# Kernel tuning notes

Hardware: AMD Instinct MI355X
Metric: run time of the kernel (lower is better)

Reference implementation:

```python
import jax, jax.numpy as jnp
import numpy as np

SCALE = 1.0 / (100.0 ** 0.5)  # module hard-codes QK / sqrt(100)


def setup_inputs() -> dict:
    key = jax.random.key(0)
    k1, k2, k3 = jax.random.split(key, 3)
    B, S, D = 8, 2048, 512
    head_size = 64
    x = jax.random.normal(k1, (B, S, D), dtype=jnp.float32)
    kernel = jax.random.normal(k2, (3, D, head_size), dtype=jnp.float32) * 0.02
    dense = jax.random.normal(k3, (D, D), dtype=jnp.float32) * 0.02
    return {"x": x, "kernel": kernel, "dense": dense, "heads": 8}


def reference(x, kernel, dense, heads):
    # All heads use the SAME kernel slices in the original loop, so each
    # iteration produces an identical V; compute once and tile.
    WQ = jnp.einsum('bsd,dh->bsh', x, kernel[0])  # [B,S,Hd]
    WK = jnp.einsum('bsd,dh->bsh', x, kernel[1])
    WV = jnp.einsum('bsd,dh->bsh', x, kernel[2])
    scores = jnp.einsum('bqh,bkh->bqk', WQ, WK) * SCALE  # [B,S,S]
    attn = jax.nn.softmax(scores, axis=-1)
    V = jnp.einsum('bqk,bkh->bqh', attn, WV)  # [B,S,Hd]
    out = jnp.tile(V, (1, 1, heads))  # concat of identical heads -> [B,S,heads*Hd]
    return jnp.einsum('bsf,fo->bso', out, dense)
```

## Files before the change

kernel.cpp:

```cpp
#include <hip/hip_runtime.h>
#include <math.h>


typedef __bf16 bf16;
typedef __bf16 bf16x4v __attribute__((ext_vector_type(4)));
typedef __bf16 bf16x8v __attribute__((ext_vector_type(8)));
typedef float f32x4 __attribute__((ext_vector_type(4)));

namespace {
constexpr int kS = 2048;
constexpr int kD = 512;
constexpr int kRows = 16384;
}

#define MFMA16(a, b, c) __builtin_amdgcn_mfma_f32_16x16x32_bf16((a), (b), (c), 0, 0, 0)

__global__ __launch_bounds__(256) void prep_kernel(const float* __restrict__ w,
                                                   const float* __restrict__ dense,
                                                   bf16* __restrict__ wtg,
                                                   bf16* __restrict__ drt) {
  const int bid = blockIdx.x, tid = threadIdx.x;
  __shared__ float T[64][65];

  if (bid < 24) {
    const int mat = bid >> 3, k0 = (bid & 7) * 64;
#pragma unroll
    for (int p = 0; p < 16; ++p) {
      int e = tid + p * 256;
      int r = e >> 6, n = e & 63;
      T[r][n] = w[mat * 32768 + (k0 + r) * 64 + n];
    }
    __syncthreads();
#pragma unroll
    for (int p = 0; p < 16; ++p) {
      int e = tid + p * 256;
      int n = e >> 6, c = e & 63;
      wtg[(size_t)mat * 32768 + (size_t)n * 512 + k0 + c] = (bf16)T[c][n];
    }
  } else {
    const int o0 = (bid - 24) * 64;
    const int oo = tid & 63, jg = tid >> 6;
    float a[16];
#pragma unroll
    for (int i = 0; i < 16; ++i) a[i] = 0.f;
#pragma unroll
    for (int h = 0; h < 8; ++h)
#pragma unroll
      for (int i = 0; i < 16; ++i)
        a[i] += dense[(size_t)(h * 64 + jg * 16 + i) * kD + o0 + oo];
#pragma unroll
    for (int i = 0; i < 16; ++i) T[oo][jg * 16 + i] = a[i];
    __syncthreads();
#pragma unroll
    for (int p = 0; p < 16; ++p) {
      int e = tid + p * 256;
      int r = e >> 6, j = e & 63;
      drt[(size_t)(o0 + r) * 64 + j] = (bf16)T[r][j];
    }
  }
}

__global__ __launch_bounds__(512) void proj_kernel(const float* __restrict__ x,
                                                   const bf16* __restrict__ wtg,
                                                   bf16* __restrict__ wq,
                                                   bf16* __restrict__ wk,
                                                   bf16* __restrict__ wvt) {
  const int bt = blockIdx.x;
  const int tid = threadIdx.x;
  const int w = tid >> 6, tx = tid & 15, quad = (tid >> 4) & 3;
  const int rt = w & 3, nh = w >> 2;
  const int row0 = bt * 64;

  __shared__ bf16 Xs[64 * 72];
  __shared__ bf16 Wts[3 * 64 * 72];

  f32x4 acc[6];
#pragma unroll
  for (int j = 0; j < 6; ++j) acc[j] = (f32x4){0.f, 0.f, 0.f, 0.f};

  const int xr0 = tid >> 4, xc4 = (tid & 15) * 4;
  const float* xb0 = &x[(size_t)(row0 + xr0) * kD + xc4];
  const float* xb1 = &x[(size_t)(row0 + xr0 + 32) * kD + xc4];
  const int wn = tid >> 3, wc8 = (tid & 7) * 8;
  const bf16* wb = &wtg[(size_t)wn * 512 + wc8];

  float4 xf0, xf1;
  uint4 wf0, wf1, wf2;
#define PROJ_ISSUE(K0)                        \
  do {                                        \
    xf0 = *(const float4*)(xb0 + (K0));       \
    xf1 = *(const float4*)(xb1 + (K0));       \
    wf0 = *(const uint4*)(wb + (K0));         \
    wf1 = *(const uint4*)(wb + 32768 + (K0)); \
    wf2 = *(const uint4*)(wb + 65536 + (K0)); \
  } while (0)

  PROJ_ISSUE(0);
  for (int k0 = 0; k0 < kD; k0 += 64) {
    __syncthreads();
    {
      bf16x4v h0 = {(bf16)xf0.x, (bf16)xf0.y, (bf16)xf0.z, (bf16)xf0.w};
      *(bf16x4v*)&Xs[xr0 * 72 + xc4] = h0;
      bf16x4v h1 = {(bf16)xf1.x, (bf16)xf1.y, (bf16)xf1.z, (bf16)xf1.w};
      *(bf16x4v*)&Xs[(xr0 + 32) * 72 + xc4] = h1;
      *(uint4*)&Wts[(0 * 64 + wn) * 72 + wc8] = wf0;
      *(uint4*)&Wts[(1 * 64 + wn) * 72 + wc8] = wf1;
      *(uint4*)&Wts[(2 * 64 + wn) * 72 + wc8] = wf2;
    }
    if (k0 + 64 < kD) PROJ_ISSUE(k0 + 64);
    __syncthreads();
#pragma unroll
    for (int s = 0; s < 2; ++s) {
      bf16x8v a = *(bf16x8v*)&Xs[(rt * 16 + tx) * 72 + s * 32 + quad * 8];
#pragma unroll
      for (int j = 0; j < 6; ++j) {
        int ntg = nh * 6 + j;
        bf16x8v bfr = *(bf16x8v*)&Wts[(ntg * 16 + tx) * 72 + s * 32 + quad * 8];
        acc[j] = MFMA16(a, bfr, acc[j]);
      }
    }
  }

#pragma unroll
  for (int j = 0; j < 6; ++j) {
    int ntg = nh * 6 + j, mat = ntg >> 2, nt = ntg & 3;
    if (mat < 2) {
      bf16* dst = mat ? wk : wq;
#pragma unroll
      for (int r = 0; r < 4; ++r) {
        int row_g = row0 + rt * 16 + quad * 4 + r;
        dst[(size_t)row_g * 64 + nt * 16 + tx] = (bf16)acc[j][r];
      }
    }
  }
  __syncthreads();
  bf16* Vt = Xs;
#pragma unroll
  for (int j = 0; j < 6; ++j) {
    int ntg = nh * 6 + j, mat = ntg >> 2, nt = ntg & 3;
    if (mat == 2) {
#pragma unroll
      for (int r = 0; r < 4; ++r)
        Vt[(nt * 16 + tx) * 72 + rt * 16 + quad * 4 + r] = (bf16)acc[j][r];
    }
  }
  __syncthreads();
  {
    int v = tid >> 3, seg = tid & 7;
    *(uint4*)&wvt[(size_t)v * kRows + row0 + seg * 8] =
        *(uint4*)&Vt[v * 72 + seg * 8];
  }
}

__global__ __launch_bounds__(512, 2) void flash_kernel(
    const bf16* __restrict__ wq, const bf16* __restrict__ wk,
    const bf16* __restrict__ wvt, const bf16* __restrict__ drt,
    float* __restrict__ out) {
  const int bid = blockIdx.x;
  const int b = bid & 7, qb = bid >> 3;
  const int q0 = qb * 32;
  const int tid = threadIdx.x;
  const int w = tid >> 6, tx = tid & 15, quad = (tid >> 4) & 3;

  __shared__ __align__(16) char lds[65536];
  __shared__ float Lsh[256];
  __shared__ __align__(16) bf16 vob[32 * 64];
  bf16* Psw = (bf16*)(lds + w * 8192);

  const bf16* wqb = wq + (size_t)(b * kS) * 64;
  const bf16* wkb = wk + (size_t)(b * kS) * 64;
  const bf16* wvb = wvt + b * kS;

  const int kc0 = (quad ^ (tx & 7)) * 8;
  const int kc1 = ((4 + quad) ^ (tx & 7)) * 8;
  const int h2 = (tx ^ (tx >> 2)) & 3;

  bf16x8v aq[2][2];
#pragma unroll
  for (int rt = 0; rt < 2; ++rt)
#pragma unroll
    for (int s = 0; s < 2; ++s)
      aq[rt][s] = *(const bf16x8v*)&wqb[(size_t)(q0 + rt * 16 + tx) * 64 +
                                        s * 32 + quad * 8];

  f32x4 oacc[2][4];
#pragma unroll
  for (int rt = 0; rt < 2; ++rt)
#pragma unroll
    for (int nt = 0; nt < 4; ++nt) oacc[rt][nt] = (f32x4){0.f, 0.f, 0.f, 0.f};
  float lsum[2][4] = {};

  const bf16* kfp = &wkb[(size_t)tx * 64 + quad * 8];
  const bf16* vfp = &wvb[(size_t)tx * kRows + quad * 8];

  for (int t = 0; t < 8; ++t) {
    const int k0 = (t * 8 + w) * 32;

    bf16x8v vb0 = *(const bf16x8v*)(vfp + (size_t)0 * 16 * kRows + k0);
    bf16x8v vb1 = *(const bf16x8v*)(vfp + (size_t)1 * 16 * kRows + k0);
    bf16x8v vb2 = *(const bf16x8v*)(vfp + (size_t)2 * 16 * kRows + k0);
    bf16x8v vb3 = *(const bf16x8v*)(vfp + (size_t)3 * 16 * kRows + k0);

#pragma unroll
    for (int nt = 0; nt < 2; ++nt) {
      const bf16* krow_p = kfp + (size_t)(k0 + nt * 16) * 64;
      bf16x8v b0 = *(const bf16x8v*)(krow_p);
      bf16x8v b1 = *(const bf16x8v*)(krow_p + 32);
#pragma unroll
      for (int rt = 0; rt < 2; ++rt) {
        f32x4 z = (f32x4){0.f, 0.f, 0.f, 0.f};
        z = MFMA16(aq[rt][0], b0, z);
        z = MFMA16(aq[rt][1], b1, z);
#pragma unroll
        for (int r = 0; r < 4; ++r) {
          float p = __expf(z[r] * 0.1f);
          lsum[rt][r] += p;
          int q = rt * 16 + quad * 4 + r;
          int chunk = nt * 2 + (tx >> 3);
          Psw[q * 32 + ((chunk ^ (r ^ quad)) * 8) + (tx & 7)] = (bf16)p;
        }
      }
    }

#pragma unroll
    for (int rt = 0; rt < 2; ++rt) {
      bf16x8v pa = *(bf16x8v*)&Psw[(rt * 16 + tx) * 32 + ((quad ^ h2) * 8)];
      oacc[rt][0] = MFMA16(pa, vb0, oacc[rt][0]);
      oacc[rt][1] = MFMA16(pa, vb1, oacc[rt][1]);
      oacc[rt][2] = MFMA16(pa, vb2, oacc[rt][2]);
      oacc[rt][3] = MFMA16(pa, vb3, oacc[rt][3]);
    }
  }

  __syncthreads();
  float* myO = (float*)(lds + w * 8192);
  float* myL = Lsh + w * 32;
#pragma unroll
  for (int rt = 0; rt < 2; ++rt)
#pragma unroll
    for (int nt = 0; nt < 4; ++nt)
#pragma unroll
      for (int r = 0; r < 4; ++r)
        myO[(rt * 16 + quad * 4 + r) * 64 + nt * 16 + tx] = oacc[rt][nt][r];
#pragma unroll
  for (int rt = 0; rt < 2; ++rt)
#pragma unroll
    for (int r = 0; r < 4; ++r) {
      float v = lsum[rt][r];
#pragma unroll
      for (int m = 1; m < 16; m <<= 1) v += __shfl_xor(v, m, 64);
      if (tx == 0) myL[rt * 16 + quad * 4 + r] = v;
    }
  __syncthreads();

#pragma unroll
  for (int p = 0; p < 4; ++p) {
    int e = tid + p * 512;
    int row = e >> 6, col = e & 63;
    float s = 0.f, lt = 0.f;
#pragma unroll
    for (int wv = 0; wv < 8; ++wv) {
      s += ((const float*)(lds + wv * 8192))[e];
      lt += Lsh[wv * 32 + row];
    }
    vob[row * 64 + (((col >> 3) ^ (row & 7)) * 8) + (col & 7)] = (bf16)(s / lt);
  }
  __syncthreads();

  bf16x8v av[2][2];
#pragma unroll
  for (int rt = 0; rt < 2; ++rt) {
    av[rt][0] = *(bf16x8v*)&vob[(rt * 16 + tx) * 64 + kc0];
    av[rt][1] = *(bf16x8v*)&vob[(rt * 16 + tx) * 64 + kc1];
  }

  float* OutS = (float*)lds;
#pragma unroll
  for (int c = 0; c < 2; ++c) {
    if (c) __syncthreads();
#pragma unroll
    for (int i = 0; i < 2; ++i) {
      const int ct = c * 16 + w * 2 + i;
      bf16x8v bd0 =
          *(const bf16x8v*)&drt[(size_t)(ct * 16 + tx) * 64 + quad * 8];
      bf16x8v bd1 =
          *(const bf16x8v*)&drt[(size_t)(ct * 16 + tx) * 64 + 32 + quad * 8];
#pragma unroll
      for (int rt = 0; rt < 2; ++rt) {
        f32x4 z = (f32x4){0.f, 0.f, 0.f, 0.f};
        z = MFMA16(av[rt][0], bd0, z);
        z = MFMA16(av[rt][1], bd1, z);
#pragma unroll
        for (int r = 0; r < 4; ++r)
          OutS[(rt * 16 + quad * 4 + r) * 260 + (w * 2 + i) * 16 + tx] = z[r];
      }
    }
    __syncthreads();
#pragma unroll
    for (int p = 0; p < 4; ++p) {
      int e = tid + p * 512;
      int row = e >> 6, seg = e & 63;
      *(float4*)&out[(size_t)(b * kS + q0 + row) * kD + c * 256 + seg * 4] =
          *(float4*)&OutS[row * 260 + seg * 4];
    }
  }
}

extern "C" void kernel_launch(void* const* d_in, const int* in_sizes, int n_in,
                              void* d_out, int out_size, void* d_ws,
                              size_t ws_size, hipStream_t stream) {
  const float* x = (const float*)d_in[0];
  const float* w = (const float*)d_in[1];
  const float* dense = (const float*)d_in[2];
  float* out = (float*)d_out;

  bf16* wq = (bf16*)d_ws;
  bf16* wk = wq + (size_t)kRows * 64;
  bf16* wvt = wk + (size_t)kRows * 64;
  bf16* wtg = wvt + (size_t)kRows * 64;
  bf16* drt = wtg + 98304;

  prep_kernel<<<32, 256, 0, stream>>>(w, dense, wtg, drt);
  proj_kernel<<<256, 512, 0, stream>>>(x, wtg, wq, wk, wvt);
  flash_kernel<<<512, 512, 0, stream>>>(wq, wk, wvt, drt, out);
}
```

Before: 140.2 us.

## Prefetch K tiles into swizzled per-wave LDS one iteration ahead

K tiles are no longer read straight from global memory into MFMA operand registers. Each wave now does coalesced 16-byte loads of the next 32-row K tile into registers while it works on the current tile, then writes them into a swizzled per-wave LDS buffer and reads MFMA fragments from there. The aim is to hide global load latency and improve coalescing. The cost is extra LDS traffic, more registers for the prefetch, and the P buffer shrinking to the upper half of each wave's LDS slot. There is no barrier between the LDS writes and the reads, which relies on each wave only ever touching its own region.

```diff
diff --git a/kernel.cpp b/kernel.cpp
--- a/kernel.cpp
+++ b/kernel.cpp
@@ -160,12 +160,13 @@
   const int b = bid & 7, qb = bid >> 3;
   const int q0 = qb * 32;
   const int tid = threadIdx.x;
-  const int w = tid >> 6, tx = tid & 15, quad = (tid >> 4) & 3;
+  const int w = tid >> 6, lane = tid & 63, tx = tid & 15, quad = (tid >> 4) & 3;
 
   __shared__ __align__(16) char lds[65536];
   __shared__ float Lsh[256];
   __shared__ __align__(16) bf16 vob[32 * 64];
-  bf16* Psw = (bf16*)(lds + w * 8192);
+  bf16* Ksw = (bf16*)(lds + w * 8192);
+  bf16* Psw = (bf16*)(lds + w * 8192 + 4096);
 
   const bf16* wqb = wq + (size_t)(b * kS) * 64;
   const bf16* wkb = wk + (size_t)(b * kS) * 64;
@@ -190,9 +191,23 @@
     for (int nt = 0; nt < 4; ++nt) oacc[rt][nt] = (f32x4){0.f, 0.f, 0.f, 0.f};
   float lsum[2][4] = {};
 
-  const bf16* kfp = &wkb[(size_t)tx * 64 + quad * 8];
+  const int ksr = lane >> 3, kslc = lane & 7;
+  const int koff = (kslc ^ ksr) * 8;
+
+  const bf16* kap = &wkb[(size_t)ksr * 64 + kslc * 8];
   const bf16* vfp = &wvb[(size_t)tx * kRows + quad * 8];
 
+  uint4 kr0, kr1, kr2, kr3;
+#define KR_ISSUE(TT)                                \
+  do {                                              \
+    const size_t kb = (size_t)(((TT)*8 + w) * 32);  \
+    kr0 = *(const uint4*)(kap + kb * 64);           \
+    kr1 = *(const uint4*)(kap + kb * 64 + 8 * 64);  \
+    kr2 = *(const uint4*)(kap + kb * 64 + 16 * 64); \
+    kr3 = *(const uint4*)(kap + kb * 64 + 24 * 64); \
+  } while (0)
+
+  KR_ISSUE(0);
   for (int t = 0; t < 8; ++t) {
     const int k0 = (t * 8 + w) * 32;
 
@@ -201,11 +216,17 @@
     bf16x8v vb2 = *(const bf16x8v*)(vfp + (size_t)2 * 16 * kRows + k0);
     bf16x8v vb3 = *(const bf16x8v*)(vfp + (size_t)3 * 16 * kRows + k0);
 
+    *(uint4*)&Ksw[(ksr + 0) * 64 + koff] = kr0;
+    *(uint4*)&Ksw[(ksr + 8) * 64 + koff] = kr1;
+    *(uint4*)&Ksw[(ksr + 16) * 64 + koff] = kr2;
+    *(uint4*)&Ksw[(ksr + 24) * 64 + koff] = kr3;
+    if (t < 7) KR_ISSUE(t + 1);
+
 #pragma unroll
     for (int nt = 0; nt < 2; ++nt) {
-      const bf16* krow_p = kfp + (size_t)(k0 + nt * 16) * 64;
-      bf16x8v b0 = *(const bf16x8v*)(krow_p);
-      bf16x8v b1 = *(const bf16x8v*)(krow_p + 32);
+      int krow = nt * 16 + tx;
+      bf16x8v b0 = *(bf16x8v*)&Ksw[krow * 64 + kc0];
+      bf16x8v b1 = *(bf16x8v*)&Ksw[krow * 64 + kc1];
 #pragma unroll
       for (int rt = 0; rt < 2; ++rt) {
         f32x4 z = (f32x4){0.f, 0.f, 0.f, 0.f};
```

Measured after the change: 132.0 us. -5.8%, faster.

## Switch flash attention inner loop to 32x32 MFMA with register-resident P

Applied to the files above, without the earlier changes.

Rewrites the attention inner loop to use 32x32x16 bf16 MFMA, computing S transposed (K as A operand) so the exponentiated probabilities can be packed to bf16 and exchanged across half-waves with shuffles instead of a round trip through LDS. K fragments for the next tile are prefetched in registers, and the output/row-sum reduction layout is adapted to the new accumulator shape. This removes per-tile LDS writes and reads of P and cuts the MFMA instruction count. In exchange it raises register pressure under the (512, 2) launch bound and makes the lane mapping more intricate.

```diff
diff --git a/kernel.cpp b/kernel.cpp
--- a/kernel.cpp
+++ b/kernel.cpp
@@ -6,6 +6,8 @@
 typedef __bf16 bf16x4v __attribute__((ext_vector_type(4)));
 typedef __bf16 bf16x8v __attribute__((ext_vector_type(8)));
 typedef float f32x4 __attribute__((ext_vector_type(4)));
+typedef float f32x16 __attribute__((ext_vector_type(16)));
+typedef unsigned int u32x4v __attribute__((ext_vector_type(4)));
 
 namespace {
 constexpr int kS = 2048;
@@ -14,6 +16,13 @@
 }
 
 #define MFMA16(a, b, c) __builtin_amdgcn_mfma_f32_16x16x32_bf16((a), (b), (c), 0, 0, 0)
+#define MFMA32(a, b, c) __builtin_amdgcn_mfma_f32_32x32x16_bf16((a), (b), (c), 0, 0, 0)
+
+static __device__ __forceinline__ unsigned pk2(float a, float b) {
+  unsigned short la = __builtin_bit_cast(unsigned short, (bf16)a);
+  unsigned short lb = __builtin_bit_cast(unsigned short, (bf16)b);
+  return (unsigned)la | ((unsigned)lb << 16);
+}
 
 __global__ __launch_bounds__(256) void prep_kernel(const float* __restrict__ w,
                                                    const float* __restrict__ dense,
@@ -160,12 +169,13 @@
   const int b = bid & 7, qb = bid >> 3;
   const int q0 = qb * 32;
   const int tid = threadIdx.x;
-  const int w = tid >> 6, tx = tid & 15, quad = (tid >> 4) & 3;
+  const int w = tid >> 6, lane = tid & 63, tx = tid & 15, quad = (tid >> 4) & 3;
+  const int tx5 = lane & 31, l5 = lane >> 5;
+  const bool hi = (l5 != 0);
 
   __shared__ __align__(16) char lds[65536];
   __shared__ float Lsh[256];
   __shared__ __align__(16) bf16 vob[32 * 64];
-  bf16* Psw = (bf16*)(lds + w * 8192);
 
   const bf16* wqb = wq + (size_t)(b * kS) * 64;
   const bf16* wkb = wk + (size_t)(b * kS) * 64;
@@ -173,97 +183,113 @@
 
   const int kc0 = (quad ^ (tx & 7)) * 8;
   const int kc1 = ((4 + quad) ^ (tx & 7)) * 8;
-  const int h2 = (tx ^ (tx >> 2)) & 3;
-
-  bf16x8v aq[2][2];
-#pragma unroll
-  for (int rt = 0; rt < 2; ++rt)
-#pragma unroll
-    for (int s = 0; s < 2; ++s)
-      aq[rt][s] = *(const bf16x8v*)&wqb[(size_t)(q0 + rt * 16 + tx) * 64 +
-                                        s * 32 + quad * 8];
-
-  f32x4 oacc[2][4];
-#pragma unroll
-  for (int rt = 0; rt < 2; ++rt)
-#pragma unroll
-    for (int nt = 0; nt < 4; ++nt) oacc[rt][nt] = (f32x4){0.f, 0.f, 0.f, 0.f};
-  float lsum[2][4] = {};
-
-  const bf16* kfp = &wkb[(size_t)tx * 64 + quad * 8];
-  const bf16* vfp = &wvb[(size_t)tx * kRows + quad * 8];
-
+
+  const bf16* qb5 = wqb + (size_t)(q0 + tx5) * 64 + l5 * 8;
+  const bf16* kb5 = wkb + (size_t)tx5 * 64 + l5 * 8;
+  const bf16* vb5 = wvb + (size_t)tx5 * kRows + l5 * 8;
+
+  bf16x8v aq0 = *(const bf16x8v*)(qb5 + 0);
+  bf16x8v aq1 = *(const bf16x8v*)(qb5 + 16);
+  bf16x8v aq2 = *(const bf16x8v*)(qb5 + 32);
+  bf16x8v aq3 = *(const bf16x8v*)(qb5 + 48);
+
+  f32x16 oacc0 = {0.f, 0.f, 0.f, 0.f, 0.f, 0.f, 0.f, 0.f,
+                  0.f, 0.f, 0.f, 0.f, 0.f, 0.f, 0.f, 0.f};
+  f32x16 oacc1 = oacc0;
+  float lsum = 0.f;
+
+  bf16x8v ka0 = *(const bf16x8v*)(kb5 + (size_t)(w * 32) * 64 + 0);
+  bf16x8v ka1 = *(const bf16x8v*)(kb5 + (size_t)(w * 32) * 64 + 16);
+  bf16x8v ka2 = *(const bf16x8v*)(kb5 + (size_t)(w * 32) * 64 + 32);
+  bf16x8v ka3 = *(const bf16x8v*)(kb5 + (size_t)(w * 32) * 64 + 48);
+
+#pragma unroll
   for (int t = 0; t < 8; ++t) {
     const int k0 = (t * 8 + w) * 32;
 
-    bf16x8v vb0 = *(const bf16x8v*)(vfp + (size_t)0 * 16 * kRows + k0);
-    bf16x8v vb1 = *(const bf16x8v*)(vfp + (size_t)1 * 16 * kRows + k0);
-    bf16x8v vb2 = *(const bf16x8v*)(vfp + (size_t)2 * 16 * kRows + k0);
-    bf16x8v vb3 = *(const bf16x8v*)(vfp + (size_t)3 * 16 * kRows + k0);
-
-#pragma unroll
-    for (int nt = 0; nt < 2; ++nt) {
-      const bf16* krow_p = kfp + (size_t)(k0 + nt * 16) * 64;
-      bf16x8v b0 = *(const bf16x8v*)(krow_p);
-      bf16x8v b1 = *(const bf16x8v*)(krow_p + 32);
-#pragma unroll
-      for (int rt = 0; rt < 2; ++rt) {
-        f32x4 z = (f32x4){0.f, 0.f, 0.f, 0.f};
-        z = MFMA16(aq[rt][0], b0, z);
-        z = MFMA16(aq[rt][1], b1, z);
-#pragma unroll
-        for (int r = 0; r < 4; ++r) {
-          float p = __expf(z[r] * 0.1f);
-          lsum[rt][r] += p;
-          int q = rt * 16 + quad * 4 + r;
-          int chunk = nt * 2 + (tx >> 3);
-          Psw[q * 32 + ((chunk ^ (r ^ quad)) * 8) + (tx & 7)] = (bf16)p;
-        }
-      }
-    }
-
-#pragma unroll
-    for (int rt = 0; rt < 2; ++rt) {
-      bf16x8v pa = *(bf16x8v*)&Psw[(rt * 16 + tx) * 32 + ((quad ^ h2) * 8)];
-      oacc[rt][0] = MFMA16(pa, vb0, oacc[rt][0]);
-      oacc[rt][1] = MFMA16(pa, vb1, oacc[rt][1]);
-      oacc[rt][2] = MFMA16(pa, vb2, oacc[rt][2]);
-      oacc[rt][3] = MFMA16(pa, vb3, oacc[rt][3]);
-    }
+    f32x16 zs = {0.f, 0.f, 0.f, 0.f, 0.f, 0.f, 0.f, 0.f,
+                 0.f, 0.f, 0.f, 0.f, 0.f, 0.f, 0.f, 0.f};
+    zs = MFMA32(ka0, aq0, zs);
+    zs = MFMA32(ka1, aq1, zs);
+    zs = MFMA32(ka2, aq2, zs);
+    zs = MFMA32(ka3, aq3, zs);
+
+    if (t < 7) {
+      const size_t kn = (size_t)((t + 1) * 8 + w) * 32 * 64;
+      ka0 = *(const bf16x8v*)(kb5 + kn + 0);
+      ka1 = *(const bf16x8v*)(kb5 + kn + 16);
+      ka2 = *(const bf16x8v*)(kb5 + kn + 32);
+      ka3 = *(const bf16x8v*)(kb5 + kn + 48);
+    }
+
+    bf16x8v vf00 = *(const bf16x8v*)(vb5 + (size_t)0 * kRows + k0 + 0);
+    bf16x8v vf01 = *(const bf16x8v*)(vb5 + (size_t)0 * kRows + k0 + 16);
+    bf16x8v vf10 = *(const bf16x8v*)(vb5 + (size_t)32 * kRows + k0 + 0);
+    bf16x8v vf11 = *(const bf16x8v*)(vb5 + (size_t)32 * kRows + k0 + 16);
+
+    float x0 = __expf(zs[0] * 0.1f), x1 = __expf(zs[1] * 0.1f);
+    float x2 = __expf(zs[2] * 0.1f), x3 = __expf(zs[3] * 0.1f);
+    float x4 = __expf(zs[4] * 0.1f), x5 = __expf(zs[5] * 0.1f);
+    float x6 = __expf(zs[6] * 0.1f), x7 = __expf(zs[7] * 0.1f);
+    float x8 = __expf(zs[8] * 0.1f), x9 = __expf(zs[9] * 0.1f);
+    float x10 = __expf(zs[10] * 0.1f), x11 = __expf(zs[11] * 0.1f);
+    float x12 = __expf(zs[12] * 0.1f), x13 = __expf(zs[13] * 0.1f);
+    float x14 = __expf(zs[14] * 0.1f), x15 = __expf(zs[15] * 0.1f);
+    lsum += (((x0 + x1) + (x2 + x3)) + ((x4 + x5) + (x6 + x7))) +
+            (((x8 + x9) + (x10 + x11)) + ((x12 + x13) + (x14 + x15)));
+
+    unsigned u0 = pk2(x0, x1);
+    unsigned u1 = pk2(x2, x3);
+    unsigned u2 = pk2(x4, x5);
+    unsigned u3 = pk2(x6, x7);
+    unsigned u4 = pk2(x8, x9);
+    unsigned u5 = pk2(x10, x11);
+    unsigned u6 = pk2(x12, x13);
+    unsigned u7 = pk2(x14, x15);
+
+    unsigned w0 = __shfl_xor(u0, 32), w1 = __shfl_xor(u1, 32);
+    unsigned w2 = __shfl_xor(u2, 32), w3 = __shfl_xor(u3, 32);
+    unsigned w4 = __shfl_xor(u4, 32), w5 = __shfl_xor(u5, 32);
+    unsigned w6 = __shfl_xor(u6, 32), w7 = __shfl_xor(u7, 32);
+    unsigned b0 = hi ? w2 : u0, b1 = hi ? w3 : u1;
+    unsigned b2 = hi ? u2 : w0, b3 = hi ? u3 : w1;
+    unsigned b4 = hi ? w6 : u4, b5 = hi ? w7 : u5;
+    unsigned b6 = hi ? u6 : w4, b7 = hi ? u7 : w5;
+    bf16x8v pb0 = __builtin_bit_cast(bf16x8v, (u32x4v){b0, b1, b2, b3});
+    bf16x8v pb1 = __builtin_bit_cast(bf16x8v, (u32x4v){b4, b5, b6, b7});
+
+    oacc0 = MFMA32(vf00, pb0, oacc0);
+    oacc0 = MFMA32(vf01, pb1, oacc0);
+    oacc1 = MFMA32(vf10, pb0, oacc1);
+    oacc1 = MFMA32(vf11, pb1, oacc1);
   }
 
   __syncthreads();
   float* myO = (float*)(lds + w * 8192);
   float* myL = Lsh + w * 32;
 #pragma unroll
-  for (int rt = 0; rt < 2; ++rt)
-#pragma unroll
-    for (int nt = 0; nt < 4; ++nt)
-#pragma unroll
-      for (int r = 0; r < 4; ++r)
-        myO[(rt * 16 + quad * 4 + r) * 64 + nt * 16 + tx] = oacc[rt][nt][r];
-#pragma unroll
-  for (int rt = 0; rt < 2; ++rt)
-#pragma unroll
-    for (int r = 0; r < 4; ++r) {
-      float v = lsum[rt][r];
-#pragma unroll
-      for (int m = 1; m < 16; m <<= 1) v += __shfl_xor(v, m, 64);
-      if (tx == 0) myL[rt * 16 + quad * 4 + r] = v;
-    }
+  for (int r = 0; r < 16; ++r) {
+    int vloc = (r & 3) + 8 * (r >> 2) + 4 * l5;
+    myO[vloc * 32 + tx5] = oacc0[r];
+    myO[(32 + vloc) * 32 + tx5] = oacc1[r];
+  }
+  {
+    float lt2 = lsum + __shfl_xor(lsum, 32);
+    if (lane < 32) myL[lane] = lt2;
+  }
   __syncthreads();
 
 #pragma unroll
   for (int p = 0; p < 4; ++p) {
     int e = tid + p * 512;
-    int row = e >> 6, col = e & 63;
+    int q = e & 31, v = e >> 5;
     float s = 0.f, lt = 0.f;
 #pragma unroll
     for (int wv = 0; wv < 8; ++wv) {
       s += ((const float*)(lds + wv * 8192))[e];
-      lt += Lsh[wv * 32 + row];
-    }
-    vob[row * 64 + (((col >> 3) ^ (row & 7)) * 8) + (col & 7)] = (bf16)(s / lt);
+      lt += Lsh[wv * 32 + q];
+    }
+    vob[q * 64 + (((v >> 3) ^ (q & 7)) * 8) + (v & 7)] = (bf16)(s / lt);
   }
   __syncthreads();
 
```

After: 133.9 us. 1.05x faster.
